# Performance work log

Hardware: AMD Instinct MI355X
Metric: run time of the kernel (lower is better)

Reference implementation:

```python
import jax, jax.numpy as jnp
import numpy as np

E = 2048
H = 16
DH = E // H  # 128
B, T = 2, 2048
EPS = 1e-8


def rmsnorm(x, g):
    rms = jnp.sqrt(jnp.mean(x * x, axis=-1, keepdims=True) + EPS)
    return g * (x / rms)


def setup_inputs() -> dict:
    key = jax.random.key(0)
    ks = jax.random.split(key, 16)
    s_in = 1.0 / np.sqrt(E)
    s_ff = 1.0 / np.sqrt(4 * E)
    return {
        "x": jax.random.normal(ks[0], (B, T, E), dtype=jnp.float32),
        # stacked per-head QKV projections, stored (in, out) so y = x @ W + b
        "wq": jax.random.normal(ks[1], (H, E, DH), dtype=jnp.float32) * s_in,
        "bq": jax.random.normal(ks[2], (H, DH), dtype=jnp.float32) * s_in,
        "wk": jax.random.normal(ks[3], (H, E, DH), dtype=jnp.float32) * s_in,
        "bk": jax.random.normal(ks[4], (H, DH), dtype=jnp.float32) * s_in,
        "wv": jax.random.normal(ks[5], (H, E, DH), dtype=jnp.float32) * s_in,
        "bv": jax.random.normal(ks[6], (H, DH), dtype=jnp.float32) * s_in,
        "wo": jax.random.normal(ks[7], (E, E), dtype=jnp.float32) * s_in,
        "bo": jax.random.normal(ks[8], (E,), dtype=jnp.float32) * s_in,
        "w1": jax.random.normal(ks[9], (E, 4 * E), dtype=jnp.float32) * s_in,
        "b1": jax.random.normal(ks[10], (4 * E,), dtype=jnp.float32) * s_in,
        "w2": jax.random.normal(ks[11], (4 * E, E), dtype=jnp.float32) * s_ff,
        "b2": jax.random.normal(ks[12], (E,), dtype=jnp.float32) * s_ff,
        "g1": jnp.ones((E,), dtype=jnp.float32),
        "g2": jnp.ones((E,), dtype=jnp.float32),
    }


def reference(x, wq, bq, wk, bk, wv, bv, wo, bo, w1, b1, w2, b2, g1, g2):
    b, t, e = x.shape
    # --- attention sublayer ---
    h = rmsnorm(x, g1)
    q = jnp.einsum("bte,hed->bhtd", h, wq) + bq[None, :, None, :]
    k = jnp.einsum("bte,hed->bhtd", h, wk) + bk[None, :, None, :]
    v = jnp.einsum("bte,hed->bhtd", h, wv) + bv[None, :, None, :]
    scores = jnp.einsum("bhtd,bhsd->bhts", q, k) / jnp.sqrt(jnp.float32(DH))
    causal = jnp.tril(jnp.ones((t, t), dtype=bool))
    scores = jnp.where(causal[None, None], scores, -jnp.inf)
    w = jax.nn.softmax(scores, axis=-1)
    o = jnp.einsum("bhts,bhsd->bhtd", w, v)
    o = o.transpose(0, 2, 1, 3).reshape(b, t, e)  # concat heads on last dim
    x = x + o @ wo + bo
    # --- FFN sublayer (exact GELU, dropout is identity at inference) ---
    h = rmsnorm(x, g2)
    x = x + jax.nn.gelu(h @ w1 + b1, approximate=False) @ w2 + b2
    return x
```

## Files before the change

### kernel.cpp

```cpp
#include <hip/hip_runtime.h>
#include <hip/hip_bf16.h>

typedef unsigned short u16;
typedef unsigned int   u32;
typedef __attribute__((ext_vector_type(8))) short short8;
typedef __attribute__((ext_vector_type(4))) float f32x4;
typedef __attribute__((ext_vector_type(4))) unsigned short u16x4;

#define E_    2048
#define H_    16
#define DH_   128
#define B_    2
#define T_    2048
#define NTOK  4096
#define QKVN  6144

#define VMCNT(n) asm volatile("s_waitcnt vmcnt(" #n ")" ::: "memory")
#define LGKM0()  asm volatile("s_waitcnt lgkmcnt(0)" ::: "memory")

__device__ __forceinline__ u16 f2bf(float f) {
  union { float f; u32 u; } v; v.f = f;
  u32 r = (v.u + 0x7FFFu + ((v.u >> 16) & 1u)) >> 16;
  return (u16)r;
}

__global__ __launch_bounds__(256) void tr64(
    const float* __restrict__ in, u16* __restrict__ out,
    int R, int C, size_t inZ, size_t outZ)
{
  __shared__ float t[64][65];
  const float* ib = in + (size_t)blockIdx.z * inZ;
  u16* ob = out + (size_t)blockIdx.z * outZ;
  const int r0 = blockIdx.y * 64, c0 = blockIdx.x * 64;
  const int tid = threadIdx.x;
  const int rr = tid >> 4;
  const int cc = (tid & 15) * 4;
  #pragma unroll
  for (int p = 0; p < 4; ++p) {
    const float4 v = *(const float4*)(ib + (size_t)(r0 + p * 16 + rr) * C + c0 + cc);
    t[cc + 0][p * 16 + rr] = v.x;
    t[cc + 1][p * 16 + rr] = v.y;
    t[cc + 2][p * 16 + rr] = v.z;
    t[cc + 3][p * 16 + rr] = v.w;
  }
  __syncthreads();
  const int wr = tid >> 3;
  const int wc = (tid & 7) * 8;
  #pragma unroll
  for (int p = 0; p < 2; ++p) {
    short8 s;
    #pragma unroll
    for (int j = 0; j < 8; ++j) s[j] = (short)f2bf(t[p * 32 + wr][wc + j]);
    *(short8*)(ob + (size_t)(c0 + p * 32 + wr) * R + r0 + wc) = s;
  }
}

__global__ __launch_bounds__(256) void bias_cat(
    const float* __restrict__ bq, const float* __restrict__ bk,
    const float* __restrict__ bv, float* __restrict__ bias)
{
  int idx = blockIdx.x * 256 + threadIdx.x;
  const float* bb = (idx < 2048) ? bq : (idx < 4096) ? bk : bv;
  bias[idx] = bb[idx & 2047];
}

__global__ __launch_bounds__(256) void rmsnorm_k(
    const float* __restrict__ x, const float* __restrict__ g, u16* __restrict__ o)
{
  const int row = blockIdx.x;
  const float4* xr = (const float4*)(x + (size_t)row * E_);
  const float4* gr = (const float4*)g;
  const int tid = threadIdx.x;
  float4 a0 = xr[tid], a1 = xr[tid + 256];
  float s = a0.x*a0.x + a0.y*a0.y + a0.z*a0.z + a0.w*a0.w
          + a1.x*a1.x + a1.y*a1.y + a1.z*a1.z + a1.w*a1.w;
  #pragma unroll
  for (int m = 1; m < 64; m <<= 1) s += __shfl_xor(s, m);
  __shared__ float wsum[4];
  if ((tid & 63) == 0) wsum[tid >> 6] = s;
  __syncthreads();
  float tot = wsum[0] + wsum[1] + wsum[2] + wsum[3];
  float rinv = rsqrtf(tot * (1.0f / E_) + 1e-8f);
  float4 g0 = gr[tid], g1 = gr[tid + 256];
  u16x4 o0, o1;
  o0[0] = f2bf(a0.x * g0.x * rinv); o0[1] = f2bf(a0.y * g0.y * rinv);
  o0[2] = f2bf(a0.z * g0.z * rinv); o0[3] = f2bf(a0.w * g0.w * rinv);
  o1[0] = f2bf(a1.x * g1.x * rinv); o1[1] = f2bf(a1.y * g1.y * rinv);
  o1[2] = f2bf(a1.z * g1.z * rinv); o1[3] = f2bf(a1.w * g1.w * rinv);
  u16x4* orow = (u16x4*)(o + (size_t)row * E_);
  orow[tid] = o0;
  orow[tid + 256] = o1;
}

__device__ __forceinline__ void gload_lds16(const void* g, u16* lds_base) {
  __builtin_amdgcn_global_load_lds(
      (const __attribute__((address_space(1))) u32*)g,
      (__attribute__((address_space(3))) u32*)lds_base, 16, 0, 0);
}

template<int MODE, int EPI>
__global__ __launch_bounds__(256, 3)
void gemm3(const u16* __restrict__ A, const u16* __restrict__ Bt,
           const float* __restrict__ bias, const float* __restrict__ resid,
           void* __restrict__ out, int M, int N, int K)
{
  constexpr int BUF = 8192;
  __shared__ __align__(16) u16 sh[3 * BUF];

  const int tid  = threadIdx.x;
  const int lane = tid & 63;
  const int l15  = lane & 15, lg = lane >> 4;
  const int w    = tid >> 6;
  const int wm   = w >> 1;
  const int wn   = w & 1;
  const int xs   = (l15 >> 1) & 3;

  const int nbx = N >> 7;
  const int xcd = blockIdx.x & 7, j = blockIdx.x >> 3;
  int m0, n0;
  if constexpr (MODE == 1) {
    const int ncx = nbx >> 3;
    n0 = (xcd * ncx + j % ncx) << 7;
    m0 = (j / ncx) << 7;
  } else {
    const int nwg = nbx * (M >> 7);
    const int sid = xcd * (nwg >> 3) + j;
    m0 = (sid / nbx) << 7;
    n0 = (sid % nbx) << 7;
  }

  const int r0 = tid >> 2;
  const int c0 = (((tid & 3) ^ ((tid >> 3) & 3)) * 8);
  const u16* gA  = A  + (size_t)(m0 + r0) * K + c0;
  const u16* gB  = Bt + (size_t)(n0 + r0) * K + c0;
  const u16* gA2 = gA + (size_t)64 * K;
  const u16* gB2 = gB + (size_t)64 * K;
  const int wub = (tid & ~63) * 8;

  f32x4 acc[4][4] = {};
  const int NT = K >> 5;

  #pragma unroll
  for (int t = 0; t < 2; ++t) {
    u16* wb = sh + t * BUF;
    const int kS = t * 32;
    gload_lds16(gA  + kS, wb + wub);
    gload_lds16(gA2 + kS, wb + 2048 + wub);
    gload_lds16(gB  + kS, wb + 4096 + wub);
    gload_lds16(gB2 + kS, wb + 6144 + wub);
  }
  VMCNT(4);
  __builtin_amdgcn_s_barrier();

  int i = 0;

#define KTILE(CUR, STG)                                                          \
  do {                                                                           \
    const u16* rb = sh + (CUR) * BUF;                                            \
    u16* wb = sh + (STG) * BUF;                                                  \
    const bool st = (i + 2 < NT);                                                \
    const int kS = (i + 2) << 5;                                                 \
    const int rem = NT - 1 - i;                                                  \
    if (st) {                                                                    \
      gload_lds16(gA  + kS, wb + wub);                                           \
      gload_lds16(gA2 + kS, wb + 2048 + wub);                                    \
      gload_lds16(gB  + kS, wb + 4096 + wub);                                    \
      gload_lds16(gB2 + kS, wb + 6144 + wub);                                    \
    }                                                                            \
    short8 af[4], bf[4];                                                         \
    _Pragma("unroll")                                                            \
    for (int n = 0; n < 4; ++n)                                                  \
      bf[n] = *(const short8*)(rb + 4096 + (wn * 64 + n * 16 + l15) * 32 + ((lg ^ xs) * 8)); \
    _Pragma("unroll")                                                            \
    for (int m = 0; m < 4; ++m)                                                  \
      af[m] = *(const short8*)(rb + (wm * 64 + m * 16 + l15) * 32 + ((lg ^ xs) * 8)); \
    _Pragma("unroll")                                                            \
    for (int m = 0; m < 4; ++m)                                                  \
      _Pragma("unroll")                                                          \
      for (int n = 0; n < 4; ++n)                                                \
        acc[m][n] = __builtin_amdgcn_mfma_f32_16x16x32_bf16(af[m], bf[n], acc[m][n], 0, 0, 0); \
    if (rem >= 2) { VMCNT(4); } else { VMCNT(0); }                               \
    __builtin_amdgcn_s_barrier();                                                \
    ++i;                                                                         \
  } while (0)

  const int trips = NT / 3;
  #pragma unroll 1
  for (int t = 0; t < trips; ++t) {
    KTILE(0, 2);
    KTILE(1, 0);
    KTILE(2, 1);
  }
  if (i < NT) KTILE(0, 2);
  if (i < NT) KTILE(1, 0);
#undef KTILE

  float bv[4];
  #pragma unroll
  for (int n = 0; n < 4; ++n) bv[n] = bias[n0 + wn * 64 + n * 16 + l15];

  if constexpr (EPI == 1) {
    #pragma unroll
    for (int n = 0; n < 4; ++n) {
      const int col = n0 + wn * 64 + n * 16 + l15;
      #pragma unroll
      for (int m = 0; m < 4; ++m)
        #pragma unroll
        for (int r = 0; r < 4; ++r) {
          const int row = m0 + wm * 64 + m * 16 + lg * 4 + r;
          const size_t off = (size_t)row * N + col;
          ((float*)out)[off] = acc[m][n][r] + bv[n] + resid[off];
        }
    }
  } else {
    u16* ep = sh + w * 1024;
    #pragma unroll
    for (int m = 0; m < 4; ++m) {
      #pragma unroll
      for (int n = 0; n < 4; ++n)
        #pragma unroll
        for (int r = 0; r < 4; ++r) {
          float v = acc[m][n][r] + bv[n];
          if (EPI == 2) {
            float t = v * (0.79788456080286536f + 0.0356774081363231f * v * v);
            v = v / (1.0f + __expf(-2.0f * t));
          }
          ep[(lg * 4 + r) * 64 + n * 16 + l15] = f2bf(v);
        }
      LGKM0();
      const int row0 = m0 + wm * 64 + m * 16;
      #pragma unroll
      for (int it = 0; it < 2; ++it) {
        const int ch = it * 64 + lane;
        const int rr = ch >> 3, c8 = ch & 7;
        short8 s = *(const short8*)(ep + rr * 64 + c8 * 8);
        *(short8*)((u16*)out + (size_t)(row0 + rr) * N + n0 + wn * 64 + c8 * 8) = s;
      }
      LGKM0();
    }
  }
}

__global__ __launch_bounds__(256) void vtrans_k(
    const u16* __restrict__ qkv, u16* __restrict__ vt)
{
  __shared__ u16 tile[DH_][66];
  const int tid = threadIdx.x;
  const int bid = blockIdx.x;
  const int tt = bid & 31;
  const int bh = bid >> 5;
  const int b  = bh >> 4, h = bh & 15;
  const int t0 = tt * 64;
  const u16* src = qkv + (size_t)b * T_ * QKVN + 2 * E_ + h * DH_;
  #pragma unroll
  for (int it = 0; it < 8; ++it) {
    int c = it * 256 + tid;
    int t = c >> 5, dc = c & 31;
    u16x4 v = *(const u16x4*)(src + (size_t)(t0 + t) * QKVN + dc * 4);
    #pragma unroll
    for (int j = 0; j < 4; ++j) tile[dc * 4 + j][t] = v[j];
  }
  __syncthreads();
  u16* dst = vt + (size_t)bh * DH_ * T_ + t0;
  #pragma unroll
  for (int it = 0; it < 8; ++it) {
    int c = it * 256 + tid;
    int d = c >> 4, tc = c & 15;
    u16x4 v;
    #pragma unroll
    for (int j = 0; j < 4; ++j) v[j] = tile[d][tc * 4 + j];
    *(u16x4*)(dst + (size_t)d * T_ + tc * 4) = v;
  }
}

__global__ __launch_bounds__(256) void attn_k(
    const u16* __restrict__ qkv, const u16* __restrict__ vt, u16* __restrict__ o)
{
  const int tid  = threadIdx.x;
  const int lane = tid & 63;
  const int w    = tid >> 6;
  const int l15  = lane & 15, lg = lane >> 4;
  const int bid  = blockIdx.x;
  const int pair = bid & 31;
  const int qt   = 15 - (bid >> 5);
  const int h    = pair & 15;
  const int b    = pair >> 4;
  const int Q0 = qt * 128;
  const int qw = Q0 + w * 32;

  __shared__ __align__(16) u16 Ks[2][64 * 128];
  __shared__ __align__(16) u16 Vs[2][128 * 64];
  __shared__ __align__(16) u16 Ps[4][32 * 64];

  const u16* qb  = qkv + (size_t)b * T_ * QKVN + h * DH_;
  const u16* kb  = qb + E_;
  const u16* vtb = vt + (size_t)(b * H_ + h) * DH_ * T_;

  short8 qf[2][4];
  #pragma unroll
  for (int qi = 0; qi < 2; ++qi)
    #pragma unroll
    for (int kk = 0; kk < 4; ++kk)
      qf[qi][kk] = *(const short8*)(qb + (size_t)(qw + qi * 16 + l15) * QKVN + kk * 32 + lg * 8);

  f32x4 oacc[2][8] = {};
  float m_[2][4], l_[2][4];
  #pragma unroll
  for (int qi = 0; qi < 2; ++qi)
    #pragma unroll
    for (int r = 0; r < 4; ++r) { m_[qi][r] = -1e30f; l_[qi][r] = 0.f; }

  const int xr = l15 & 7;
  const float scl = 0.08838834764831845f;
  const int nt = Q0 / 64 + 2;
  const int qmaxw = qw + 31;
  const int wub = (tid & ~63);

  const u16* kp[4]; const u16* vp[4];
  #pragma unroll
  for (int i = 0; i < 4; ++i) {
    int f = i * 256 + tid;
    int r = f >> 4, p = f & 15, c = p ^ (r & 7);
    kp[i] = kb + (size_t)r * QKVN + c * 8;
  }
  #pragma unroll
  for (int i = 0; i < 4; ++i) {
    int f = i * 256 + tid;
    int d = f >> 3, p = f & 7, c = p ^ (d & 7);
    vp[i] = vtb + (size_t)d * T_ + c * 8;
  }

  auto STAGEKV = [&](int s0, int bufi) {
    const size_t ko = (size_t)s0 * QKVN;
    #pragma unroll
    for (int i = 0; i < 4; ++i)
      gload_lds16(kp[i] + ko, &Ks[bufi][(i * 256 + wub) * 8]);
    #pragma unroll
    for (int i = 0; i < 4; ++i)
      gload_lds16(vp[i] + s0, &Vs[bufi][(i * 256 + wub) * 8]);
  };

  STAGEKV(0, 0);
  VMCNT(0);
  __builtin_amdgcn_s_barrier();

  #pragma unroll 1
  for (int st = 0; st < nt; ++st) {
    const int s0 = st * 64;
    const int cur = st & 1;
    if (st + 1 < nt) STAGEKV(s0 + 64, cur ^ 1);

    if (s0 <= qmaxw) {
      const u16* Kc = Ks[cur];
      const u16* Vc = Vs[cur];
      f32x4 sc[2][4] = {};
      __builtin_amdgcn_s_setprio(1);
      #pragma unroll
      for (int sj = 0; sj < 4; ++sj) {
        const int row = sj * 16 + l15;
        #pragma unroll
        for (int kk = 0; kk < 4; ++kk) {
          short8 kfr = *(const short8*)(Kc + row * 128 + (((kk * 4 + lg) ^ xr) * 8));
          sc[0][sj] = __builtin_amdgcn_mfma_f32_16x16x32_bf16(qf[0][kk], kfr, sc[0][sj], 0, 0, 0);
          sc[1][sj] = __builtin_amdgcn_mfma_f32_16x16x32_bf16(qf[1][kk], kfr, sc[1][sj], 0, 0, 0);
        }
      }
      __builtin_amdgcn_s_setprio(0);
      const bool needmask = (s0 + 63 > qw);
      #pragma unroll
      for (int qi = 0; qi < 2; ++qi)
        #pragma unroll
        for (int sj = 0; sj < 4; ++sj)
          #pragma unroll
          for (int r = 0; r < 4; ++r) {
            float v = sc[qi][sj][r] * scl;
            if (needmask) {
              int s = s0 + sj * 16 + l15;
              int q = qw + qi * 16 + lg * 4 + r;
              if (s > q) v = -1e30f;
            }
            sc[qi][sj][r] = v;
          }
      #pragma unroll
      for (int qi = 0; qi < 2; ++qi) {
        float tmax[4], alpha[4], rsum[4];
        #pragma unroll
        for (int r = 0; r < 4; ++r)
          tmax[r] = fmaxf(fmaxf(sc[qi][0][r], sc[qi][1][r]), fmaxf(sc[qi][2][r], sc[qi][3][r]));
        #pragma unroll
        for (int r = 0; r < 4; ++r)
          #pragma unroll
          for (int m = 1; m < 16; m <<= 1) tmax[r] = fmaxf(tmax[r], __shfl_xor(tmax[r], m));
        #pragma unroll
        for (int r = 0; r < 4; ++r) {
          float mn = fmaxf(m_[qi][r], tmax[r]);
          alpha[r] = __expf(m_[qi][r] - mn);
          m_[qi][r] = mn;
          rsum[r] = 0.f;
        }
        #pragma unroll
        for (int sj = 0; sj < 4; ++sj)
          #pragma unroll
          for (int r = 0; r < 4; ++r) {
            float p = __expf(sc[qi][sj][r] - m_[qi][r]);
            rsum[r] += p;
            const int row = qi * 16 + lg * 4 + r;
            const int ch  = (sj * 2 + (l15 >> 3)) ^ (row & 7);
            Ps[w][row * 64 + ch * 8 + (l15 & 7)] = f2bf(p);
          }
        #pragma unroll
        for (int r = 0; r < 4; ++r) {
          #pragma unroll
          for (int m = 1; m < 16; m <<= 1) rsum[r] += __shfl_xor(rsum[r], m);
          l_[qi][r] = l_[qi][r] * alpha[r] + rsum[r];
        }
        #pragma unroll
        for (int dj = 0; dj < 8; ++dj)
          #pragma unroll
          for (int r = 0; r < 4; ++r) oacc[qi][dj][r] *= alpha[r];
      }
      __builtin_amdgcn_s_setprio(1);
      #pragma unroll
      for (int ks = 0; ks < 2; ++ks) {
        short8 pf0 = *(const short8*)(&Ps[w][l15 * 64 + (((ks * 4 + lg) ^ xr) * 8)]);
        short8 pf1 = *(const short8*)(&Ps[w][(16 + l15) * 64 + (((ks * 4 + lg) ^ xr) * 8)]);
        #pragma unroll
        for (int dj = 0; dj < 8; ++dj) {
          const int row = dj * 16 + l15;
          short8 vfr = *(const short8*)(Vc + row * 64 + (((ks * 4 + lg) ^ xr) * 8));
          oacc[0][dj] = __builtin_amdgcn_mfma_f32_16x16x32_bf16(pf0, vfr, oacc[0][dj], 0, 0, 0);
          oacc[1][dj] = __builtin_amdgcn_mfma_f32_16x16x32_bf16(pf1, vfr, oacc[1][dj], 0, 0, 0);
        }
      }
      __builtin_amdgcn_s_setprio(0);
    }
    VMCNT(0);
    __builtin_amdgcn_s_barrier();
  }

  float inv[2][4];
  #pragma unroll
  for (int qi = 0; qi < 2; ++qi)
    #pragma unroll
    for (int r = 0; r < 4; ++r) inv[qi][r] = 1.0f / l_[qi][r];
  u16* ob = o + (size_t)(b * T_ + qw) * E_ + h * DH_;
  #pragma unroll
  for (int qi = 0; qi < 2; ++qi)
    #pragma unroll
    for (int dj = 0; dj < 8; ++dj)
      #pragma unroll
      for (int r = 0; r < 4; ++r)
        ob[(size_t)(qi * 16 + lg * 4 + r) * E_ + dj * 16 + l15] = f2bf(oacc[qi][dj][r] * inv[qi][r]);
}

extern "C" void kernel_launch(void* const* d_in, const int* in_sizes, int n_in,
                              void* d_out, int out_size, void* d_ws, size_t ws_size,
                              hipStream_t stream)
{
  const float* x  = (const float*)d_in[0];
  const float* wq = (const float*)d_in[1];
  const float* bq = (const float*)d_in[2];
  const float* wk = (const float*)d_in[3];
  const float* bk = (const float*)d_in[4];
  const float* wv = (const float*)d_in[5];
  const float* bv = (const float*)d_in[6];
  const float* wo = (const float*)d_in[7];
  const float* bo = (const float*)d_in[8];
  const float* w1 = (const float*)d_in[9];
  const float* b1 = (const float*)d_in[10];
  const float* w2 = (const float*)d_in[11];
  const float* b2 = (const float*)d_in[12];
  const float* g1 = (const float*)d_in[13];
  const float* g2 = (const float*)d_in[14];
  float* xout = (float*)d_out;

  if (ws_size < 201351168u) return;

  char* ws = (char*)d_ws;
  u16*   wqkv_t = (u16*)(ws + 0);
  u16*   h1     = (u16*)(ws + 25165824);
  u16*   qkv    = (u16*)(ws + 41943040);
  u16*   vt     = (u16*)(ws + 92274688);
  u16*   o_     = (u16*)(ws + 109051904);
  u16*   wo_t   = (u16*)(ws + 125829120);
  u16*   w1_t   = (u16*)(ws + 134217728);
  u16*   w2_t   = (u16*)(ws + 167772160);
  float* bqkv   = (float*)(ws + 201326592);
  u16*   u_     = (u16*)(ws + 0);
  u16*   h2     = vt;
  float* x2     = xout;

  tr64<<<dim3(2, 32, 16), 256, 0, stream>>>(wq, wqkv_t,                          E_, DH_, (size_t)E_ * DH_, (size_t)DH_ * E_);
  tr64<<<dim3(2, 32, 16), 256, 0, stream>>>(wk, wqkv_t + (size_t)E_ * E_,        E_, DH_, (size_t)E_ * DH_, (size_t)DH_ * E_);
  tr64<<<dim3(2, 32, 16), 256, 0, stream>>>(wv, wqkv_t + (size_t)2 * E_ * E_,    E_, DH_, (size_t)E_ * DH_, (size_t)DH_ * E_);
  tr64<<<dim3(32, 32, 1),  256, 0, stream>>>(wo, wo_t, E_, E_, 0, 0);
  tr64<<<dim3(128, 32, 1), 256, 0, stream>>>(w1, w1_t, E_, 4 * E_, 0, 0);
  tr64<<<dim3(32, 128, 1), 256, 0, stream>>>(w2, w2_t, 4 * E_, E_, 0, 0);
  bias_cat<<<24, 256, 0, stream>>>(bq, bk, bv, bqkv);

  rmsnorm_k<<<NTOK, 256, 0, stream>>>(x, g1, h1);
  gemm3<1, 0><<<(NTOK / 128) * (QKVN / 128), 256, 0, stream>>>(h1, wqkv_t, bqkv, nullptr, qkv, NTOK, QKVN, E_);
  vtrans_k<<<B_ * H_ * (T_ / 64), 256, 0, stream>>>(qkv, vt);
  attn_k<<<B_ * H_ * (T_ / 16 / 8), 256, 0, stream>>>(qkv, vt, o_);
  gemm3<0, 1><<<(NTOK / 128) * (E_ / 128), 256, 0, stream>>>(o_, wo_t, bo, x, x2, NTOK, E_, E_);
  rmsnorm_k<<<NTOK, 256, 0, stream>>>(x2, g2, h2);
  gemm3<1, 2><<<(NTOK / 128) * (4 * E_ / 128), 256, 0, stream>>>(h2, w1_t, b1, nullptr, u_, NTOK, 4 * E_, E_);
  gemm3<0, 1><<<(NTOK / 128) * (E_ / 128), 256, 0, stream>>>(u_, w2_t, b2, x2, xout, NTOK, E_, 4 * E_);
}
```

Before: 689.3 us.

## Fuse V transpose into QKV GEMM, double-buffer small GEMM, add 256x256 FFN1 GEMM

The 128x128 GEMM now uses two LDS buffers instead of three and raises occupancy via launch bounds of 5 blocks, waiting for all loads each k-step. Its new epilogue mode writes the V columns transposed straight into the vt buffer, which removes the separate vtrans kernel. A new 512-thread 256x256-tile GEMM with triple buffering handles the FFN up-projection to get more operand reuse. The trade-offs are less load/compute overlap in the small GEMM and fewer workgroups for the large one.

```diff
diff --git a/kernel.cpp b/kernel.cpp
--- a/kernel.cpp
+++ b/kernel.cpp
@@ -99,13 +99,12 @@
 }
 
 template<int MODE, int EPI>
-__global__ __launch_bounds__(256, 3)
-void gemm3(const u16* __restrict__ A, const u16* __restrict__ Bt,
+__global__ __launch_bounds__(256, 5)
+void gemmA(const u16* __restrict__ A, const u16* __restrict__ Bt,
            const float* __restrict__ bias, const float* __restrict__ resid,
-           void* __restrict__ out, int M, int N, int K)
+           void* __restrict__ out, u16* __restrict__ vtout, int M, int N, int K)
 {
-  constexpr int BUF = 8192;
-  __shared__ __align__(16) u16 sh[3 * BUF];
+  __shared__ __align__(16) u16 sh[2 * 8192];
 
   const int tid  = threadIdx.x;
   const int lane = tid & 63;
@@ -140,28 +139,21 @@
   f32x4 acc[4][4] = {};
   const int NT = K >> 5;
 
-  #pragma unroll
-  for (int t = 0; t < 2; ++t) {
-    u16* wb = sh + t * BUF;
-    const int kS = t * 32;
-    gload_lds16(gA  + kS, wb + wub);
-    gload_lds16(gA2 + kS, wb + 2048 + wub);
-    gload_lds16(gB  + kS, wb + 4096 + wub);
-    gload_lds16(gB2 + kS, wb + 6144 + wub);
-  }
-  VMCNT(4);
+  gload_lds16(gA,  sh + wub);
+  gload_lds16(gA2, sh + 2048 + wub);
+  gload_lds16(gB,  sh + 4096 + wub);
+  gload_lds16(gB2, sh + 6144 + wub);
+  VMCNT(0);
   __builtin_amdgcn_s_barrier();
 
   int i = 0;
 
-#define KTILE(CUR, STG)                                                          \
+#define KTILE(CUR)                                                               \
   do {                                                                           \
-    const u16* rb = sh + (CUR) * BUF;                                            \
-    u16* wb = sh + (STG) * BUF;                                                  \
-    const bool st = (i + 2 < NT);                                                \
-    const int kS = (i + 2) << 5;                                                 \
-    const int rem = NT - 1 - i;                                                  \
-    if (st) {                                                                    \
+    const u16* rb = sh + (CUR) * 8192;                                           \
+    u16* wb = sh + (1 - (CUR)) * 8192;                                           \
+    if (i + 1 < NT) {                                                            \
+      const int kS = (i + 1) << 5;                                               \
       gload_lds16(gA  + kS, wb + wub);                                           \
       gload_lds16(gA2 + kS, wb + 2048 + wub);                                    \
       gload_lds16(gB  + kS, wb + 4096 + wub);                                    \
@@ -179,20 +171,17 @@
       _Pragma("unroll")                                                          \
       for (int n = 0; n < 4; ++n)                                                \
         acc[m][n] = __builtin_amdgcn_mfma_f32_16x16x32_bf16(af[m], bf[n], acc[m][n], 0, 0, 0); \
-    if (rem >= 2) { VMCNT(4); } else { VMCNT(0); }                               \
+    VMCNT(0);                                                                    \
     __builtin_amdgcn_s_barrier();                                                \
     ++i;                                                                         \
   } while (0)
 
-  const int trips = NT / 3;
+  const int trips = NT >> 1;
   #pragma unroll 1
   for (int t = 0; t < trips; ++t) {
-    KTILE(0, 2);
-    KTILE(1, 0);
-    KTILE(2, 1);
-  }
-  if (i < NT) KTILE(0, 2);
-  if (i < NT) KTILE(1, 0);
+    KTILE(0);
+    KTILE(1);
+  }
 #undef KTILE
 
   float bv[4];
@@ -211,6 +200,30 @@
           const size_t off = (size_t)row * N + col;
           ((float*)out)[off] = acc[m][n][r] + bv[n] + resid[off];
         }
+    }
+  } else if (EPI == 3 && n0 >= 4096) {
+    u16* epb = sh + w * 4096;
+    #pragma unroll
+    for (int n = 0; n < 4; ++n)
+      #pragma unroll
+      for (int m = 0; m < 4; ++m)
+        #pragma unroll
+        for (int r = 0; r < 4; ++r)
+          epb[(n * 16 + l15) * 64 + m * 16 + lg * 4 + r] = f2bf(acc[m][n][r] + bv[n]);
+    LGKM0();
+    const int colV0 = n0 - 4096 + wn * 64;
+    const int hh = colV0 >> 7;
+    const int db = colV0 & 127;
+    const int tw = m0 + wm * 64;
+    const int bb = tw >> 11;
+    const int tb = tw & 2047;
+    u16* vbase = vtout + ((size_t)(bb * 16 + hh) * 128 + db) * 2048 + tb;
+    #pragma unroll
+    for (int it = 0; it < 8; ++it) {
+      const int c = it * 64 + lane;
+      const int d = c >> 3, sl = c & 7;
+      short8 s = *(const short8*)(epb + d * 64 + sl * 8);
+      *(short8*)(vbase + (size_t)d * 2048 + sl * 8) = s;
     }
   } else {
     u16* ep = sh + w * 1024;
@@ -241,35 +254,150 @@
   }
 }
 
-__global__ __launch_bounds__(256) void vtrans_k(
-    const u16* __restrict__ qkv, u16* __restrict__ vt)
+template<int MODE, int EPI>
+__global__ __launch_bounds__(512, 2)
+void gemmB(const u16* __restrict__ A, const u16* __restrict__ Bt,
+           const float* __restrict__ bias, const float* __restrict__ resid,
+           void* __restrict__ out, int M, int N, int K)
 {
-  __shared__ u16 tile[DH_][66];
-  const int tid = threadIdx.x;
-  const int bid = blockIdx.x;
-  const int tt = bid & 31;
-  const int bh = bid >> 5;
-  const int b  = bh >> 4, h = bh & 15;
-  const int t0 = tt * 64;
-  const u16* src = qkv + (size_t)b * T_ * QKVN + 2 * E_ + h * DH_;
-  #pragma unroll
-  for (int it = 0; it < 8; ++it) {
-    int c = it * 256 + tid;
-    int t = c >> 5, dc = c & 31;
-    u16x4 v = *(const u16x4*)(src + (size_t)(t0 + t) * QKVN + dc * 4);
-    #pragma unroll
-    for (int j = 0; j < 4; ++j) tile[dc * 4 + j][t] = v[j];
-  }
-  __syncthreads();
-  u16* dst = vt + (size_t)bh * DH_ * T_ + t0;
-  #pragma unroll
-  for (int it = 0; it < 8; ++it) {
-    int c = it * 256 + tid;
-    int d = c >> 4, tc = c & 15;
-    u16x4 v;
-    #pragma unroll
-    for (int j = 0; j < 4; ++j) v[j] = tile[d][tc * 4 + j];
-    *(u16x4*)(dst + (size_t)d * T_ + tc * 4) = v;
+  constexpr int BUF = 16384;
+  __shared__ __align__(16) u16 sh[3 * BUF];
+
+  const int tid  = threadIdx.x;
+  const int lane = tid & 63;
+  const int l15  = lane & 15, lg = lane >> 4;
+  const int w    = tid >> 6;
+  const int wm   = w >> 2;
+  const int wn   = w & 3;
+  const int xs   = (l15 >> 1) & 3;
+
+  const int nbx = N >> 8;
+  const int xcd = blockIdx.x & 7, j = blockIdx.x >> 3;
+  int m0, n0;
+  if constexpr (MODE == 1) {
+    const int ncx = nbx >> 3;
+    n0 = (xcd * ncx + j % ncx) << 8;
+    m0 = (j / ncx) << 8;
+  } else {
+    const int nwg = nbx * (M >> 8);
+    const int sid = xcd * (nwg >> 3) + j;
+    m0 = (sid / nbx) << 8;
+    n0 = (sid % nbx) << 8;
+  }
+
+  const int r0 = tid >> 2;
+  const int c0 = (((tid & 3) ^ ((tid >> 3) & 3)) * 8);
+  const u16* gA  = A  + (size_t)(m0 + r0) * K + c0;
+  const u16* gB  = Bt + (size_t)(n0 + r0) * K + c0;
+  const u16* gA2 = gA + (size_t)128 * K;
+  const u16* gB2 = gB + (size_t)128 * K;
+  const int wub = (tid & ~63) * 8;
+
+  f32x4 acc[8][4] = {};
+  const int NT = K >> 5;
+
+  #pragma unroll
+  for (int t = 0; t < 2; ++t) {
+    u16* wb = sh + t * BUF;
+    const int kS = t * 32;
+    gload_lds16(gA  + kS, wb + wub);
+    gload_lds16(gA2 + kS, wb + 4096 + wub);
+    gload_lds16(gB  + kS, wb + 8192 + wub);
+    gload_lds16(gB2 + kS, wb + 12288 + wub);
+  }
+  VMCNT(4);
+  __builtin_amdgcn_s_barrier();
+
+  int i = 0;
+
+#define KTILE(CUR, STG)                                                          \
+  do {                                                                           \
+    const u16* rb = sh + (CUR) * BUF;                                            \
+    u16* wb = sh + (STG) * BUF;                                                  \
+    const bool st = (i + 2 < NT);                                                \
+    const int kS = (i + 2) << 5;                                                 \
+    const int rem = NT - 1 - i;                                                  \
+    if (st) {                                                                    \
+      gload_lds16(gA  + kS, wb + wub);                                           \
+      gload_lds16(gA2 + kS, wb + 4096 + wub);                                    \
+      gload_lds16(gB  + kS, wb + 8192 + wub);                                    \
+      gload_lds16(gB2 + kS, wb + 12288 + wub);                                   \
+    }                                                                            \
+    short8 bf[4];                                                                \
+    _Pragma("unroll")                                                            \
+    for (int n = 0; n < 4; ++n)                                                  \
+      bf[n] = *(const short8*)(rb + 8192 + (wn * 64 + n * 16 + l15) * 32 + ((lg ^ xs) * 8)); \
+    _Pragma("unroll")                                                            \
+    for (int mh = 0; mh < 2; ++mh) {                                             \
+      short8 af[4];                                                              \
+      _Pragma("unroll")                                                          \
+      for (int m = 0; m < 4; ++m)                                                \
+        af[m] = *(const short8*)(rb + (wm * 128 + (mh * 4 + m) * 16 + l15) * 32 + ((lg ^ xs) * 8)); \
+      _Pragma("unroll")                                                          \
+      for (int m = 0; m < 4; ++m)                                                \
+        _Pragma("unroll")                                                        \
+        for (int n = 0; n < 4; ++n)                                              \
+          acc[mh * 4 + m][n] = __builtin_amdgcn_mfma_f32_16x16x32_bf16(af[m], bf[n], acc[mh * 4 + m][n], 0, 0, 0); \
+    }                                                                            \
+    if (rem >= 2) { VMCNT(4); } else { VMCNT(0); }                               \
+    __builtin_amdgcn_s_barrier();                                                \
+    ++i;                                                                         \
+  } while (0)
+
+  const int trips = NT / 3;
+  #pragma unroll 1
+  for (int t = 0; t < trips; ++t) {
+    KTILE(0, 2);
+    KTILE(1, 0);
+    KTILE(2, 1);
+  }
+  if (i < NT) KTILE(0, 2);
+  if (i < NT) KTILE(1, 0);
+#undef KTILE
+
+  float bv[4];
+  #pragma unroll
+  for (int n = 0; n < 4; ++n) bv[n] = bias[n0 + wn * 64 + n * 16 + l15];
+
+  if constexpr (EPI == 1) {
+    #pragma unroll
+    for (int n = 0; n < 4; ++n) {
+      const int col = n0 + wn * 64 + n * 16 + l15;
+      #pragma unroll
+      for (int m = 0; m < 8; ++m)
+        #pragma unroll
+        for (int r = 0; r < 4; ++r) {
+          const int row = m0 + wm * 128 + m * 16 + lg * 4 + r;
+          const size_t off = (size_t)row * N + col;
+          ((float*)out)[off] = acc[m][n][r] + bv[n] + resid[off];
+        }
+    }
+  } else {
+    u16* ep = sh + w * 1024;
+    #pragma unroll
+    for (int m = 0; m < 8; ++m) {
+      #pragma unroll
+      for (int n = 0; n < 4; ++n)
+        #pragma unroll
+        for (int r = 0; r < 4; ++r) {
+          float v = acc[m][n][r] + bv[n];
+          if (EPI == 2) {
+            float t = v * (0.79788456080286536f + 0.0356774081363231f * v * v);
+            v = v / (1.0f + __expf(-2.0f * t));
+          }
+          ep[(lg * 4 + r) * 64 + n * 16 + l15] = f2bf(v);
+        }
+      LGKM0();
+      const int row0 = m0 + wm * 128 + m * 16;
+      #pragma unroll
+      for (int it = 0; it < 2; ++it) {
+        const int ch = it * 64 + lane;
+        const int rr = ch >> 3, c8 = ch & 7;
+        short8 s = *(const short8*)(ep + rr * 64 + c8 * 8);
+        *(short8*)((u16*)out + (size_t)(row0 + rr) * N + n0 + wn * 64 + c8 * 8) = s;
+      }
+      LGKM0();
+    }
   }
 }
 
@@ -499,11 +627,10 @@
   bias_cat<<<24, 256, 0, stream>>>(bq, bk, bv, bqkv);
 
   rmsnorm_k<<<NTOK, 256, 0, stream>>>(x, g1, h1);
-  gemm3<1, 0><<<(NTOK / 128) * (QKVN / 128), 256, 0, stream>>>(h1, wqkv_t, bqkv, nullptr, qkv, NTOK, QKVN, E_);
-  vtrans_k<<<B_ * H_ * (T_ / 64), 256, 0, stream>>>(qkv, vt);
+  gemmA<1, 3><<<(NTOK / 128) * (QKVN / 128), 256, 0, stream>>>(h1, wqkv_t, bqkv, nullptr, qkv, vt, NTOK, QKVN, E_);
   attn_k<<<B_ * H_ * (T_ / 16 / 8), 256, 0, stream>>>(qkv, vt, o_);
-  gemm3<0, 1><<<(NTOK / 128) * (E_ / 128), 256, 0, stream>>>(o_, wo_t, bo, x, x2, NTOK, E_, E_);
+  gemmA<0, 1><<<(NTOK / 128) * (E_ / 128), 256, 0, stream>>>(o_, wo_t, bo, x, x2, nullptr, NTOK, E_, E_);
   rmsnorm_k<<<NTOK, 256, 0, stream>>>(x2, g2, h2);
-  gemm3<1, 2><<<(NTOK / 128) * (4 * E_ / 128), 256, 0, stream>>>(h2, w1_t, b1, nullptr, u_, NTOK, 4 * E_, E_);
-  gemm3<0, 1><<<(NTOK / 128) * (E_ / 128), 256, 0, stream>>>(u_, w2_t, b2, x2, xout, NTOK, E_, 4 * E_);
-}
+  gemmB<1, 2><<<(NTOK / 256) * (4 * E_ / 256), 512, 0, stream>>>(h2, w1_t, b1, nullptr, u_, NTOK, 4 * E_, E_);
+  gemmA<0, 1><<<(NTOK / 128) * (E_ / 128), 256, 0, stream>>>(u_, w2_t, b2, x2, xout, nullptr, NTOK, E_, 4 * E_);
+}
```

New measurement: 918.4 us. 33.2% more time.
